# Kernel tuning notes

Measured on AMD Instinct MI355X. Metric: run time of the kernel, lower is better.

Reference implementation:

```python
import jax, jax.numpy as jnp
import numpy as np

EPS = 1e-05
KERNEL_SIZE = 9
KERNEL_VOL = float(KERNEL_SIZE ** 3)

_DN = ("NDHWC", "DHWIO", "NDHWC")


def _box_sum(x, k=KERNEL_SIZE):
    """Sliding-window sum over a k^3 box with SAME zero padding.

    The TF module uses a dense all-ones (k,k,k) conv3d; an all-ones kernel is
    separable, so three 1D passes compute the identical result with O(k) work.
    x: (B, D1, D2, D3, 1) float.
    """
    for kshape in ((k, 1, 1), (1, k, 1), (1, 1, k)):
        w = jnp.ones(kshape + (1, 1), dtype=x.dtype)
        x = jax.lax.conv_general_dilated(
            x, w, window_strides=(1, 1, 1), padding="SAME",
            dimension_numbers=_DN)
    return x


def setup_inputs() -> dict:
    key = jax.random.key(0)
    k1, k2 = jax.random.split(key)
    shape = (2, 192, 192, 192)
    y_true = jax.random.uniform(k1, shape, dtype=jnp.float32)
    y_pred = jax.random.uniform(k2, shape, dtype=jnp.float32)
    return {"y_true": y_true, "y_pred": y_pred}


def reference(y_true, y_pred):
    # Expand (B, D1, D2, D3) -> (B, D1, D2, D3, 1) as in the TF call().
    if y_true.ndim == 4:
        y_true = y_true[..., None]
        y_pred = y_pred[..., None]

    t_sum = _box_sum(y_true)
    p_sum = _box_sum(y_pred)
    tp_sum = _box_sum(y_true * y_pred)

    t_avg = t_sum / KERNEL_VOL
    p_avg = p_sum / KERNEL_VOL

    cross = tp_sum - p_avg * t_sum
    num = cross * cross + EPS  # the DEBUG1 variant returns `num` directly
    return num
```

## Files before the change

### kernel.cpp

```cpp
#include <hip/hip_runtime.h>


#define N 192
#define RSTRIDE 46

#define LDS_BARRIER() asm volatile("s_waitcnt lgkmcnt(0)\n\ts_barrier" ::: "memory")

__global__ __launch_bounds__(1024, 4)
void lncc_kernel(const float* __restrict__ t_in,
                 const float* __restrict__ p_in,
                 float* __restrict__ out)
{
    __shared__ __align__(16) float rowT[3 * 32 * RSTRIDE];
    __shared__ float pcol[3 * 32 * 32];

    const int bid = blockIdx.x;
    int xy, Z, z0;
    if (bid < 64) {
        xy = bid >> 3;
        Z  = 24;
        z0 = (bid & 7) * 24;
    } else {
        const int q  = bid - 64;
        xy = 8 + q / 7;
        const int zi = q % 7;
        if (zi < 3) { Z = 28; z0 = zi * 28; }
        else        { Z = 27; z0 = 84 + (zi - 3) * 27; }
    }
    const int b  = xy / 36;
    const int t6 = xy % 36;
    const int y0 = (t6 / 6) * 32, x0 = (t6 % 6) * 32;
    const int tid = threadIdx.x;

    const int  lf   = tid / 320;
    const int  ls   = tid - lf * 320;
    const int  lry  = ls >> 3;
    const int  lxq  = ls & 7;
    const int  lgy  = y0 - 4 + lry;
    const int  lgx0 = x0 - 4 + 4 * lxq;
    const bool lactive = (tid < 960);
    const bool lyok = ((unsigned)lgy < (unsigned)N);

    const int  cf  = tid >> 8;
    const int  cyq = (tid >> 5) & 7;
    const int  cx  = tid & 31;
    const bool cactive = (tid < 768);

    const int gx = tid & 31;
    const int gy = tid >> 5;

    const size_t plane = (size_t)N * N;
    const float* tb = t_in + (size_t)b * N * plane;
    const float* pb = p_in + (size_t)b * N * plane;
    float*       ob = out  + (size_t)b * N * plane
                           + (size_t)(y0 + gy) * N + (x0 + gx);

    const int lgyc = lyok ? lgy : 0;
    const float* const trow = tb + (size_t)lgyc * N;
    const float* const prow = pb + (size_t)lgyc * N;
    const float* const arow = (lf == 1) ? prow : trow;

    float ring_t[9], ring_p[9], ring_tp[9];
    float sum_t = 0.f, sum_p = 0.f, sum_tp = 0.f;
    #pragma unroll
    for (int i = 0; i < 9; ++i) { ring_t[i] = 0.f; ring_p[i] = 0.f; ring_tp[i] = 0.f; }

    const float4 z4 = make_float4(0.f, 0.f, 0.f, 0.f);
    float4 cur0 = z4, cur1 = z4, cur2 = z4;

    {
        const int zp0 = z0 - 4;
        if (((unsigned)zp0 < (unsigned)N) && lactive && lyok) {
            const float* ar = arow + (size_t)zp0 * plane;
            const float* cr = prow + (size_t)zp0 * plane;
            float4 a[3], c[3];
            #pragma unroll
            for (int q = 0; q < 3; ++q) {
                a[q] = z4; c[q] = z4;
                const int gxq = lgx0 + 4 * q;
                if ((unsigned)gxq < (unsigned)N) {
                    a[q] = *(const float4*)(ar + gxq);
                    if (lf == 2) c[q] = *(const float4*)(cr + gxq);
                }
            }
            if (lf == 2) {
                #pragma unroll
                for (int q = 0; q < 3; ++q) {
                    a[q].x *= c[q].x; a[q].y *= c[q].y;
                    a[q].z *= c[q].z; a[q].w *= c[q].w;
                }
            }
            cur0 = a[0]; cur1 = a[1]; cur2 = a[2];
        }
    }

    #pragma unroll 1
    for (int k = 0; k < 4; ++k) {
      #pragma unroll
      for (int r = 0; r < 9; ++r) {
        const int i  = k * 9 + r;
        const int zp = z0 - 4 + i;
        const int zn = zp + 1;
        const bool vi = (i < Z + 8)     && ((unsigned)zp < (unsigned)N);
        const bool vn = (i + 1 < Z + 8) && ((unsigned)zn < (unsigned)N);

        float4 fa0 = z4, fa1 = z4, fa2 = z4, fc0 = z4, fc1 = z4, fc2 = z4;
        if (vn && lactive && lyok) {
            const float* ar = arow + (size_t)zn * plane;
            const float* cr = prow + (size_t)zn * plane;
            const int g0 = lgx0, g1 = lgx0 + 4, g2 = lgx0 + 8;
            if ((unsigned)g0 < (unsigned)N) {
                fa0 = *(const float4*)(ar + g0);
                if (lf == 2) fc0 = *(const float4*)(cr + g0);
            }
            if ((unsigned)g1 < (unsigned)N) {
                fa1 = *(const float4*)(ar + g1);
                if (lf == 2) fc1 = *(const float4*)(cr + g1);
            }
            if ((unsigned)g2 < (unsigned)N) {
                fa2 = *(const float4*)(ar + g2);
                if (lf == 2) fc2 = *(const float4*)(cr + g2);
            }
        }

        if (vi && lactive) {
            const float v0 = cur0.x, v1 = cur0.y, v2  = cur0.z, v3  = cur0.w;
            const float v4 = cur1.x, v5 = cur1.y, v6  = cur1.z, v7  = cur1.w;
            const float v8 = cur2.x, v9 = cur2.y, v10 = cur2.z, v11 = cur2.w;
            float s0 = ((v0+v1) + (v2+v3)) + ((v4+v5) + (v6+v7)) + v8;
            float s1 = s0 - v0 + v9;
            float s2 = s1 - v1 + v10;
            float s3 = s2 - v2 + v11;
            float* wp = &rowT[(lf * 32 + 4 * lxq) * RSTRIDE + lry];
            wp[0]           = s0;
            wp[RSTRIDE]     = s1;
            wp[2 * RSTRIDE] = s2;
            wp[3 * RSTRIDE] = s3;
        }
        LDS_BARRIER();

        if (vi && cactive) {
            const float* rb = &rowT[(cf * 32 + cx) * RSTRIDE + 4 * cyq];
            const float2 u0 = *(const float2*)(rb + 0);
            const float2 u1 = *(const float2*)(rb + 2);
            const float2 u2 = *(const float2*)(rb + 4);
            const float2 u3 = *(const float2*)(rb + 6);
            const float2 u4 = *(const float2*)(rb + 8);
            const float2 u5 = *(const float2*)(rb + 10);
            const float w0=u0.x, w1=u0.y, w2=u1.x,  w3=u1.y;
            const float w4=u2.x, w5=u2.y, w6=u3.x,  w7=u3.y;
            const float w8=u4.x, w9=u4.y, w10=u5.x, w11=u5.y;
            float c0 = ((w0+w1)+(w2+w3)) + ((w4+w5)+(w6+w7)) + w8;
            float c1 = c0 - w0 + w9;
            float c2 = c1 - w1 + w10;
            float c3 = c2 - w2 + w11;
            float* pc = &pcol[cf * 1024 + (4 * cyq) * 32 + cx];
            pc[0]  = c0;
            pc[32] = c1;
            pc[64] = c2;
            pc[96] = c3;
        }
        LDS_BARRIER();

        float Pt = 0.f, Pp = 0.f, Ptp = 0.f;
        if (vi) {
            Pt  = pcol[       gy * 32 + gx];
            Pp  = pcol[1024 + gy * 32 + gx];
            Ptp = pcol[2048 + gy * 32 + gx];
        }
        sum_t  += Pt  - ring_t[r];  ring_t[r]  = Pt;
        sum_p  += Pp  - ring_p[r];  ring_p[r]  = Pp;
        sum_tp += Ptp - ring_tp[r]; ring_tp[r] = Ptp;
        if (i >= 8 && i < Z + 8) {
            const float cross = sum_tp - (sum_p * (1.0f / 729.0f)) * sum_t;
            ob[(size_t)(z0 + i - 8) * plane] = cross * cross + 1e-5f;
        }

        if (vn && lactive) {
            float4 A0 = fa0, A1 = fa1, A2 = fa2;
            if (lf == 2) {
                A0.x *= fc0.x; A0.y *= fc0.y; A0.z *= fc0.z; A0.w *= fc0.w;
                A1.x *= fc1.x; A1.y *= fc1.y; A1.z *= fc1.z; A1.w *= fc1.w;
                A2.x *= fc2.x; A2.y *= fc2.y; A2.z *= fc2.z; A2.w *= fc2.w;
            }
            cur0 = A0; cur1 = A1; cur2 = A2;
        }
      }
    }
}

extern "C" void kernel_launch(void* const* d_in, const int* in_sizes, int n_in,
                              void* d_out, int out_size, void* d_ws, size_t ws_size,
                              hipStream_t stream) {
    const float* y_true = (const float*)d_in[0];
    const float* y_pred = (const float*)d_in[1];
    float* out = (float*)d_out;
    dim3 grid(512);
    dim3 block(1024);
    hipLaunchKernelGGL(lncc_kernel, grid, block, 0, stream, y_true, y_pred, out);
}
```

Before: 210.3 us.

## Retile to 24x32 xy tiles with longer z runs and 768-thread blocks

Changes the block decomposition from 32x32 xy tiles with z chunks of 24-28 slices to 24x32 tiles with z chunks of 38-39 slices, using 480 blocks of 768 threads. All 768 threads now load rows and 576 of them do the column pass, where before 64 of the 1024 threads sat idle in the load phase and 256 in the column pass. Longer z runs amortise the 8-slice z halo over more output slices. The shorter y tile raises the y-halo share, and the row-stride padding in LDS is reduced to match.

```diff
diff --git a/kernel.cpp b/kernel.cpp
--- a/kernel.cpp
+++ b/kernel.cpp
@@ -2,49 +2,43 @@
 
 
 #define N 192
-#define RSTRIDE 46
+#define RSTRIDE 34
 
 #define LDS_BARRIER() asm volatile("s_waitcnt lgkmcnt(0)\n\ts_barrier" ::: "memory")
 
-__global__ __launch_bounds__(1024, 4)
+__global__ __launch_bounds__(768, 2)
 void lncc_kernel(const float* __restrict__ t_in,
                  const float* __restrict__ p_in,
                  float* __restrict__ out)
 {
     __shared__ __align__(16) float rowT[3 * 32 * RSTRIDE];
-    __shared__ float pcol[3 * 32 * 32];
+    __shared__ float pcol[3 * 24 * 32];
 
     const int bid = blockIdx.x;
-    int xy, Z, z0;
-    if (bid < 64) {
-        xy = bid >> 3;
-        Z  = 24;
-        z0 = (bid & 7) * 24;
-    } else {
-        const int q  = bid - 64;
-        xy = 8 + q / 7;
-        const int zi = q % 7;
-        if (zi < 3) { Z = 28; z0 = zi * 28; }
-        else        { Z = 27; z0 = 84 + (zi - 3) * 27; }
-    }
-    const int b  = xy / 36;
-    const int t6 = xy % 36;
-    const int y0 = (t6 / 6) * 32, x0 = (t6 % 6) * 32;
+    const int xy  = bid / 5;
+    const int zi  = bid % 5;
+    const int Z   = (zi < 2) ? 39 : 38;
+    const int z0  = (zi < 2) ? zi * 39 : 78 + (zi - 2) * 38;
+
+    const int b  = xy / 48;
+    const int t6 = xy % 48;
+    const int y0 = (t6 / 6) * 24;
+    const int x0 = (t6 % 6) * 32;
     const int tid = threadIdx.x;
 
-    const int  lf   = tid / 320;
-    const int  ls   = tid - lf * 320;
+    const int  lf   = tid >> 8;
+    const int  ls   = tid & 255;
     const int  lry  = ls >> 3;
     const int  lxq  = ls & 7;
     const int  lgy  = y0 - 4 + lry;
     const int  lgx0 = x0 - 4 + 4 * lxq;
-    const bool lactive = (tid < 960);
     const bool lyok = ((unsigned)lgy < (unsigned)N);
 
-    const int  cf  = tid >> 8;
-    const int  cyq = (tid >> 5) & 7;
-    const int  cx  = tid & 31;
-    const bool cactive = (tid < 768);
+    const int  cf  = tid / 192;
+    const int  cs  = tid - cf * 192;
+    const int  cyq = cs >> 5;
+    const int  cx  = cs & 31;
+    const bool cactive = (tid < 576);
 
     const int gx = tid & 31;
     const int gy = tid >> 5;
@@ -70,7 +64,7 @@
 
     {
         const int zp0 = z0 - 4;
-        if (((unsigned)zp0 < (unsigned)N) && lactive && lyok) {
+        if (((unsigned)zp0 < (unsigned)N) && lyok) {
             const float* ar = arow + (size_t)zp0 * plane;
             const float* cr = prow + (size_t)zp0 * plane;
             float4 a[3], c[3];
@@ -95,17 +89,18 @@
     }
 
     #pragma unroll 1
-    for (int k = 0; k < 4; ++k) {
+    for (int k = 0; k < 6; ++k) {
       #pragma unroll
       for (int r = 0; r < 9; ++r) {
         const int i  = k * 9 + r;
+        if (i >= Z + 8) break;
         const int zp = z0 - 4 + i;
         const int zn = zp + 1;
-        const bool vi = (i < Z + 8)     && ((unsigned)zp < (unsigned)N);
+        const bool vi = ((unsigned)zp < (unsigned)N);
         const bool vn = (i + 1 < Z + 8) && ((unsigned)zn < (unsigned)N);
 
         float4 fa0 = z4, fa1 = z4, fa2 = z4, fc0 = z4, fc1 = z4, fc2 = z4;
-        if (vn && lactive && lyok) {
+        if (vn && lyok) {
             const float* ar = arow + (size_t)zn * plane;
             const float* cr = prow + (size_t)zn * plane;
             const int g0 = lgx0, g1 = lgx0 + 4, g2 = lgx0 + 8;
@@ -123,7 +118,7 @@
             }
         }
 
-        if (vi && lactive) {
+        if (vi) {
             const float v0 = cur0.x, v1 = cur0.y, v2  = cur0.z, v3  = cur0.w;
             const float v4 = cur1.x, v5 = cur1.y, v6  = cur1.z, v7  = cur1.w;
             const float v8 = cur2.x, v9 = cur2.y, v10 = cur2.z, v11 = cur2.w;
@@ -154,7 +149,7 @@
             float c1 = c0 - w0 + w9;
             float c2 = c1 - w1 + w10;
             float c3 = c2 - w2 + w11;
-            float* pc = &pcol[cf * 1024 + (4 * cyq) * 32 + cx];
+            float* pc = &pcol[cf * 768 + (4 * cyq) * 32 + cx];
             pc[0]  = c0;
             pc[32] = c1;
             pc[64] = c2;
@@ -165,18 +160,18 @@
         float Pt = 0.f, Pp = 0.f, Ptp = 0.f;
         if (vi) {
             Pt  = pcol[       gy * 32 + gx];
-            Pp  = pcol[1024 + gy * 32 + gx];
-            Ptp = pcol[2048 + gy * 32 + gx];
+            Pp  = pcol[ 768 + gy * 32 + gx];
+            Ptp = pcol[1536 + gy * 32 + gx];
         }
         sum_t  += Pt  - ring_t[r];  ring_t[r]  = Pt;
         sum_p  += Pp  - ring_p[r];  ring_p[r]  = Pp;
         sum_tp += Ptp - ring_tp[r]; ring_tp[r] = Ptp;
-        if (i >= 8 && i < Z + 8) {
+        if (i >= 8) {
             const float cross = sum_tp - (sum_p * (1.0f / 729.0f)) * sum_t;
             ob[(size_t)(z0 + i - 8) * plane] = cross * cross + 1e-5f;
         }
 
-        if (vn && lactive) {
+        if (vn) {
             float4 A0 = fa0, A1 = fa1, A2 = fa2;
             if (lf == 2) {
                 A0.x *= fc0.x; A0.y *= fc0.y; A0.z *= fc0.z; A0.w *= fc0.w;
@@ -195,7 +190,7 @@
     const float* y_true = (const float*)d_in[0];
     const float* y_pred = (const float*)d_in[1];
     float* out = (float*)d_out;
-    dim3 grid(512);
-    dim3 block(1024);
+    dim3 grid(480);
+    dim3 block(768);
     hipLaunchKernelGGL(lncc_kernel, grid, block, 0, stream, y_true, y_pred, out);
 }
```

Result: slower. 222.0 us (+5.6%).
